# Kernel tuning notes

Measured on AMD Instinct MI355X. Metric: run time of the kernel, lower is better.

Reference implementation:

```python
import jax, jax.numpy as jnp
import numpy as np

CUTOFF = 0.05

def _freq_filter(x_chw, filter_type):
    # x_chw: [C,H,W] = batch element 0, detached in the original (stop_gradient)
    x = jax.lax.stop_gradient(x_chw)
    C, H, W = x.shape
    a = jnp.abs(x)
    mn = a.min(axis=(1, 2), keepdims=True)
    ptp = a.max(axis=(1, 2), keepdims=True) - mn
    # np.uint8(255*(a-mn)/ptp): values in [0,255], cast truncates -> floor
    q = jnp.floor(255.0 * (a - mn) / ptp)
    f = jnp.fft.fftshift(jnp.fft.fft2(q), axes=(-2, -1))
    crow, ccol = H // 2, W // 2
    dr, dc = int(CUTOFF * crow), int(CUTOFF * ccol)
    m = jnp.zeros((H, W), dtype=q.dtype)
    m = m.at[crow - dr:crow + dr, ccol - dc:ccol + dc].set(1.0)
    if filter_type == 'low_pass':
        m = 1.0 - m  # note: original 'low_pass' actually removes low freqs
    out = jnp.abs(jnp.fft.ifft2(jnp.fft.ifftshift(f * m, axes=(-2, -1))))
    return out.astype(x_chw.dtype)  # [C,H,W]

def _conv1x1(x, w, b):
    # x: [B,C,H,W], w: [O,C], b: [O]
    return jnp.einsum('oc,bchw->bohw', w, x) + b[None, :, None, None]

def setup_inputs() -> dict:
    key = jax.random.key(0)
    ks = jax.random.split(key, 7)
    B, C, H, W = 1, 256, 96, 96
    fuse = jax.random.normal(ks[0], (B, C, H, W), dtype=jnp.float32)
    s = 1.0 / np.sqrt(C)
    Wq = jax.random.normal(ks[1], (C, C), dtype=jnp.float32) * s
    bq = jax.random.normal(ks[2], (C,), dtype=jnp.float32) * 0.01
    Wk = jax.random.normal(ks[3], (C, C), dtype=jnp.float32) * s
    bk = jax.random.normal(ks[4], (C,), dtype=jnp.float32) * 0.01
    Wv = jax.random.normal(ks[5], (C, C), dtype=jnp.float32) * s
    bv = jax.random.normal(ks[6], (C,), dtype=jnp.float32) * 0.01
    return {"fuse": fuse, "Wq": Wq, "bq": bq, "Wk": Wk, "bk": bk, "Wv": Wv, "bv": bv}

def reference(fuse, Wq, bq, Wk, bk, Wv, bv):
    B, C, H, W = fuse.shape
    scale = 1.0 / (C ** 0.5)
    # frequency-filtered maps (computed from batch 0, broadcast to all batches)
    FQ = jnp.broadcast_to(_freq_filter(fuse[0], 'high_pass'), fuse.shape)
    FK = jnp.broadcast_to(_freq_filter(fuse[0], 'low_pass'), fuse.shape)
    fuse_Query = _conv1x1(FQ, Wq, bq).reshape(B, C, H * W)     # [B,C,HW]
    fuse_Q_mask = fuse_Query.reshape(B * H, C * W)             # [B*H, C*W]
    fuse_Query_t = jnp.transpose(fuse_Query, (0, 2, 1))        # [B,HW,C]
    fuse_Key = _conv1x1(FK, Wk, bk).reshape(B, C, H * W)       # [B,C,HW]
    Fuse_Q_mask = jnp.max(fuse_Q_mask, axis=0, keepdims=True)  # [1, C*W]
    mask_KQ = jnp.einsum('bnc,bcm->bnm', fuse_Query_t, fuse_Key) * scale  # [B,HW,HW]
    mask_KQ = jax.nn.softmax(mask_KQ, axis=0)  # softmax over batch dim (as in original)
    mask_KQ = jnp.max(mask_KQ, axis=1)                         # [B,HW]
    mask_KQ = mask_KQ.reshape(-1, W)                           # [B*H, W]
    mask_KQ = jnp.max(mask_KQ, axis=-1, keepdims=True)         # [B*H, 1]
    mask = (mask_KQ @ Fuse_Q_mask).reshape(B, C, H, W)
    fuse_Value = _conv1x1(fuse, Wv, bv)
    return fuse_Value + fuse_Value * mask
```

## Files before the change

kernel.cpp:

```cpp
#include <hip/hip_runtime.h>
#include <math.h>

#define CCH 256
#define HW  9216
#define CW  24576
#define TWO_PI 6.28318530717958647692f

typedef __attribute__((ext_vector_type(8))) short short8;
typedef __attribute__((ext_vector_type(4))) float f32x4;

__device__ inline unsigned short f2bf(float f) {
    unsigned u = __float_as_uint(f);
    unsigned r = (u + 0x7FFFu + ((u >> 16) & 1u)) >> 16;
    return (unsigned short)r;
}

__global__ __launch_bounds__(256) void k_wf(const float* __restrict__ Wq,
                                            const float* __restrict__ Wv,
                                            short8* __restrict__ Wqt,
                                            short8* __restrict__ Wvt,
                                            unsigned* __restrict__ FQm) {
    int widx = blockIdx.x;
    int t = threadIdx.x;
    int z0 = widx * 384;
    FQm[z0 + t] = 0u;
    if (t < 128) FQm[z0 + 256 + t] = 0u;
    const float* src = (widx >= 32) ? Wv : Wq;
    short8* dst = (widx >= 32) ? Wvt : Wqt;
    int cidx = (widx & 31) * 256 + t;
    int ot = cidx >> 11, kc = (cidx >> 6) & 31, m = cidx & 63;
    const float* s = src + (ot * 64 + m) * 256 + kc * 8;
    short8 v;
    #pragma unroll
    for (int e = 0; e < 8; ++e) v[e] = (short)f2bf(s[e]);
    dst[cidx] = v;
}

__global__ __launch_bounds__(768) void k_dft(const float* __restrict__ x,
                                             float* __restrict__ Fg) {
    __shared__ float qa[HW];
    __shared__ float cs[96][2];
    __shared__ float Gp[8][96][5];
    __shared__ float Gs[96][6];
    __shared__ float red[24];
    __shared__ float s_mn, s_ptp;
    int c = blockIdx.x, t = threadIdx.x;
    const float* xp = x + c * HW;
    if (t < 96) { float a = TWO_PI * (float)t / 96.0f; cs[t][0] = cosf(a); cs[t][1] = sinf(a); }
    float lo = 1e30f, hi = 0.f;
    #pragma unroll
    for (int i = 0; i < 12; ++i) {
        float a = fabsf(xp[t + i * 768]);
        qa[t + i * 768] = a;
        lo = fminf(lo, a);
        hi = fmaxf(hi, a);
    }
    #pragma unroll
    for (int d = 32; d; d >>= 1) {
        lo = fminf(lo, __shfl_xor(lo, d, 64));
        hi = fmaxf(hi, __shfl_xor(hi, d, 64));
    }
    if ((t & 63) == 0) { red[t >> 6] = lo; red[12 + (t >> 6)] = hi; }
    __syncthreads();
    if (t == 0) {
        lo = red[0]; hi = red[12];
        #pragma unroll
        for (int i = 1; i < 12; ++i) { lo = fminf(lo, red[i]); hi = fmaxf(hi, red[12 + i]); }
        s_mn = lo; s_ptp = hi - lo;
    }
    __syncthreads();
    float mn = s_mn, ptp = s_ptp;

    {
        int xx = t % 96, h = t / 96;
        float g0r = 0, g0i = 0, g1r = 0, g1i = 0, g2 = 0;
        for (int y = h * 12; y < h * 12 + 12; ++y) {
            float q = floorf(255.0f * (qa[y * 96 + xx] - mn) / ptp);
            float c1 = cs[y][0], s1 = cs[y][1];
            float c2 = c1 * c1 - s1 * s1, s2 = 2.0f * c1 * s1;
            g0r += q * c2; g0i += q * s2;
            g1r += q * c1; g1i += q * s1;
            g2  += q;
        }
        Gp[h][xx][0] = g0r; Gp[h][xx][1] = g0i;
        Gp[h][xx][2] = g1r; Gp[h][xx][3] = g1i;
        Gp[h][xx][4] = g2;
    }
    __syncthreads();
    if (t < 96) {
        #pragma unroll
        for (int j = 0; j < 5; ++j) {
            float s = 0.f;
            #pragma unroll
            for (int h = 0; h < 8; ++h) s += Gp[h][t][j];
            Gs[t][j] = s;
        }
        Gs[t][5] = 0.f;
    }
    __syncthreads();
    if (t < 64) {
        int coef = t >> 2, qq = t & 3;
        int ky = coef >> 2, kx = coef & 3;
        float fr = 0, fi = 0;
        for (int xx = qq * 24; xx < qq * 24 + 24; ++xx) {
            float c1 = cs[xx][0], s1 = cs[xx][1];
            float er, ei;
            if (kx == 0)      { er = c1 * c1 - s1 * s1; ei = 2.0f * c1 * s1; }
            else if (kx == 1) { er = c1; ei = s1; }
            else if (kx == 2) { er = 1.f; ei = 0.f; }
            else              { er = c1; ei = -s1; }
            float gr, gi;
            if (ky == 0)      { gr = Gs[xx][0]; gi = Gs[xx][1]; }
            else if (ky == 1) { gr = Gs[xx][2]; gi = Gs[xx][3]; }
            else if (ky == 2) { gr = Gs[xx][4]; gi = 0.f; }
            else              { gr = Gs[xx][2]; gi = -Gs[xx][3]; }
            fr += gr * er - gi * ei;
            fi += gr * ei + gi * er;
        }
        fr += __shfl_xor(fr, 1, 64); fr += __shfl_xor(fr, 2, 64);
        fi += __shfl_xor(fi, 1, 64); fi += __shfl_xor(fi, 2, 64);
        if (qq == 0) {
            Fg[c * 32 + 2 * coef]     = fr;
            Fg[c * 32 + 2 * coef + 1] = fi;
        }
    }
}

__global__ __launch_bounds__(256) void k_gemm1(const short8* __restrict__ Wt,
                                               const float* __restrict__ Fg,
                                               const float* __restrict__ bias,
                                               unsigned* __restrict__ FQm) {
    __shared__ short8 As[2048];
    __shared__ short8 Bs[2048];
    __shared__ float Rs[2048][2];
    int tid = threadIdx.x;
    int pt_ = blockIdx.x, ot = blockIdx.y;
    const short8* wsrc = Wt + ot * 2048;
    #pragma unroll
    for (int i = 0; i < 8; ++i) As[i * 256 + tid] = wsrc[i * 256 + tid];

    int p0 = pt_ * 64;
    int y0 = p0 / 96;
    {
        int yi = (tid >> 2) & 1, kx = tid & 3, cb = tid >> 3;
        float ay = TWO_PI * (float)(y0 + yi) / 96.0f;
        float cyv = cosf(ay), syv = sinf(ay);
        float cy2 = cyv * cyv - syv * syv, sy2 = 2.f * cyv * syv;
        float Ur[4] = { cy2, cyv, 1.f, cyv };
        float Ui[4] = { -sy2, -syv, 0.f, syv };
        #pragma unroll
        for (int i = 0; i < 8; ++i) {
            int cc = cb + i * 32;
            float rr = 0.f, ri = 0.f;
            #pragma unroll
            for (int ky = 0; ky < 4; ++ky) {
                float fr = Fg[cc * 32 + 2 * (ky * 4 + kx)];
                float fi = Fg[cc * 32 + 2 * (ky * 4 + kx) + 1];
                rr += fr * Ur[ky] - fi * Ui[ky];
                ri += fr * Ui[ky] + fi * Ur[ky];
            }
            Rs[cc * 8 + yi * 4 + kx][0] = rr;
            Rs[cc * 8 + yi * 4 + kx][1] = ri;
        }
    }
    __syncthreads();
    const float inv = 1.0f / 9216.0f;
    #pragma unroll
    for (int i = 0; i < 8; ++i) {
        int si = i * 256 + tid;
        int kcg = si >> 6, n = si & 63;
        int p = p0 + n;
        int y = p / 96, xx = p - y * 96;
        int yi = y - y0;
        float axv = TWO_PI * (float)xx / 96.0f;
        float cxv = cosf(axv), sxv = sinf(axv);
        float cx2 = cxv * cxv - sxv * sxv, sx2 = 2.f * cxv * sxv;
        float Tr[4] = { cx2, cxv, 1.f, cxv };
        float Ti[4] = { -sx2, -sxv, 0.f, sxv };
        short8 vv;
        #pragma unroll
        for (int e = 0; e < 8; ++e) {
            int rb = (kcg * 8 + e) * 8 + yi * 4;
            float ar = 0.f, ai = 0.f;
            #pragma unroll
            for (int kx = 0; kx < 4; ++kx) {
                float rr = Rs[rb + kx][0], ri = Rs[rb + kx][1];
                ar += rr * Tr[kx] - ri * Ti[kx];
                ai += rr * Ti[kx] + ri * Tr[kx];
            }
            vv[e] = (short)f2bf(sqrtf(ar * ar + ai * ai) * inv);
        }
        Bs[si] = vv;
    }
    __syncthreads();

    int l = tid & 63, w = tid >> 6;
    int wr = w >> 1, wc = w & 1;
    int l15 = l & 15, quad = l >> 4;
    f32x4 acc[2][2] = {};
    int abase = wr * 32 + l15;
    int bbase = wc * 32 + l15;
    #pragma unroll
    for (int s = 0; s < 8; ++s) {
        int kc = s * 4 + quad;
        short8 a0 = As[kc * 64 + abase];
        short8 a1 = As[kc * 64 + abase + 16];
        short8 b0 = Bs[kc * 64 + bbase];
        short8 b1 = Bs[kc * 64 + bbase + 16];
        acc[0][0] = __builtin_amdgcn_mfma_f32_16x16x32_bf16(a0, b0, acc[0][0], 0, 0, 0);
        acc[0][1] = __builtin_amdgcn_mfma_f32_16x16x32_bf16(a0, b1, acc[0][1], 0, 0, 0);
        acc[1][0] = __builtin_amdgcn_mfma_f32_16x16x32_bf16(a1, b0, acc[1][0], 0, 0, 0);
        acc[1][1] = __builtin_amdgcn_mfma_f32_16x16x32_bf16(a1, b1, acc[1][1], 0, 0, 0);
    }
    #pragma unroll
    for (int ni = 0; ni < 2; ++ni) {
        #pragma unroll
        for (int r = 0; r < 4; ++r) {
            int o_lo = ot * 64 + wr * 32 + quad * 4 + r;
            float v = fmaxf(acc[0][ni][r] + bias[o_lo], acc[1][ni][r] + bias[o_lo + 16]);
            v = fmaxf(v, __shfl_xor(v, 32, 64));
            if (quad < 2) {
                int p = pt_ * 64 + wc * 32 + ni * 16 + l15;
                int k = ((quad * 4 + r) & 7) * HW + p;
                if (k >= CW) k -= CW;
                if (k >= CW) k -= CW;
                unsigned u = __float_as_uint(v);
                unsigned key = (u & 0x80000000u) ? ~u : (u | 0x80000000u);
                atomicMax(&FQm[k], key);
            }
        }
    }
}

__global__ __launch_bounds__(256) void k_gemm2(const short8* __restrict__ Wt,
                                               const float* __restrict__ x,
                                               const float* __restrict__ bias,
                                               const unsigned* __restrict__ FQm,
                                               float* __restrict__ out) {
    __shared__ short8 As[2048];
    __shared__ short8 Bs[2048];
    __shared__ unsigned short lt[64][66];
    int tid = threadIdx.x;
    int pt_ = blockIdx.x, ot = blockIdx.y;
    const short8* wsrc = Wt + ot * 2048;
    #pragma unroll
    for (int i = 0; i < 8; ++i) As[i * 256 + tid] = wsrc[i * 256 + tid];

    int p0 = pt_ * 64;
    int tx = tid & 63, tw = tid >> 6;
    for (int ct4 = 0; ct4 < 4; ++ct4) {
        #pragma unroll
        for (int i = 0; i < 16; ++i) {
            int row = tw * 16 + i;
            lt[row][tx] = f2bf(x[(size_t)(ct4 * 64 + row) * HW + p0 + tx]);
        }
        __syncthreads();
        #pragma unroll
        for (int ch = 0; ch < 2; ++ch) {
            int lc = ch * 256 + tid;
            int kcg = lc >> 6, n = lc & 63;
            short8 v;
            #pragma unroll
            for (int e = 0; e < 8; ++e) v[e] = (short)lt[kcg * 8 + e][n];
            Bs[(ct4 * 8 + kcg) * 64 + n] = v;
        }
        __syncthreads();
    }

    int l = tid & 63, w = tid >> 6;
    int wr = w >> 1, wc = w & 1;
    int l15 = l & 15, quad = l >> 4;
    f32x4 acc[2][2] = {};
    int abase = wr * 32 + l15;
    int bbase = wc * 32 + l15;
    #pragma unroll
    for (int s = 0; s < 8; ++s) {
        int kc = s * 4 + quad;
        short8 a0 = As[kc * 64 + abase];
        short8 a1 = As[kc * 64 + abase + 16];
        short8 b0 = Bs[kc * 64 + bbase];
        short8 b1 = Bs[kc * 64 + bbase + 16];
        acc[0][0] = __builtin_amdgcn_mfma_f32_16x16x32_bf16(a0, b0, acc[0][0], 0, 0, 0);
        acc[0][1] = __builtin_amdgcn_mfma_f32_16x16x32_bf16(a0, b1, acc[0][1], 0, 0, 0);
        acc[1][0] = __builtin_amdgcn_mfma_f32_16x16x32_bf16(a1, b0, acc[1][0], 0, 0, 0);
        acc[1][1] = __builtin_amdgcn_mfma_f32_16x16x32_bf16(a1, b1, acc[1][1], 0, 0, 0);
    }
    #pragma unroll
    for (int mi = 0; mi < 2; ++mi) {
        #pragma unroll
        for (int ni = 0; ni < 2; ++ni) {
            #pragma unroll
            for (int r = 0; r < 4; ++r) {
                int o = ot * 64 + wr * 32 + mi * 16 + quad * 4 + r;
                int p = pt_ * 64 + wc * 32 + ni * 16 + l15;
                int k = ((quad * 4 + r) & 7) * HW + p;
                if (k >= CW) k -= CW;
                if (k >= CW) k -= CW;
                unsigned key = FQm[k];
                unsigned ub = (key & 0x80000000u) ? (key ^ 0x80000000u) : ~key;
                float m = __uint_as_float(ub);
                float v = acc[mi][ni][r] + bias[o];
                out[(size_t)o * HW + p] = v * (1.0f + m);
            }
        }
    }
}

extern "C" void kernel_launch(void* const* d_in, const int* in_sizes, int n_in,
                              void* d_out, int out_size, void* d_ws, size_t ws_size,
                              hipStream_t stream) {
    const float* fuse = (const float*)d_in[0];
    const float* Wq   = (const float*)d_in[1];
    const float* bq   = (const float*)d_in[2];
    const float* Wv   = (const float*)d_in[5];
    const float* bv   = (const float*)d_in[6];
    float* out = (float*)d_out;

    char* ws = (char*)d_ws;
    unsigned* FQm = (unsigned*)(ws);
    float*    Fg  = (float*)(ws + 98304);
    short8*   Wqt = (short8*)(ws + 131072);
    short8*   Wvt = (short8*)(ws + 262144);

    k_wf<<<64, 256, 0, stream>>>(Wq, Wv, Wqt, Wvt, FQm);
    k_dft<<<256, 768, 0, stream>>>(fuse, Fg);
    k_gemm1<<<dim3(144, 4), 256, 0, stream>>>(Wqt, Fg, bq, FQm);
    k_gemm2<<<dim3(144, 4), 256, 0, stream>>>(Wvt, fuse, bv, FQm, out);
}
```

Measured before the change: 120.1 us.

## Merge weight-prep into DFT kernel and load gemm2 B tile directly

Result: faster. 115.6 us (-3.8%).

```diff
diff --git a/kernel.cpp b/kernel.cpp
--- a/kernel.cpp
+++ b/kernel.cpp
@@ -15,28 +15,12 @@
     return (unsigned short)r;
 }
 
-__global__ __launch_bounds__(256) void k_wf(const float* __restrict__ Wq,
-                                            const float* __restrict__ Wv,
-                                            short8* __restrict__ Wqt,
-                                            short8* __restrict__ Wvt,
-                                            unsigned* __restrict__ FQm) {
-    int widx = blockIdx.x;
-    int t = threadIdx.x;
-    int z0 = widx * 384;
-    FQm[z0 + t] = 0u;
-    if (t < 128) FQm[z0 + 256 + t] = 0u;
-    const float* src = (widx >= 32) ? Wv : Wq;
-    short8* dst = (widx >= 32) ? Wvt : Wqt;
-    int cidx = (widx & 31) * 256 + t;
-    int ot = cidx >> 11, kc = (cidx >> 6) & 31, m = cidx & 63;
-    const float* s = src + (ot * 64 + m) * 256 + kc * 8;
-    short8 v;
-    #pragma unroll
-    for (int e = 0; e < 8; ++e) v[e] = (short)f2bf(s[e]);
-    dst[cidx] = v;
-}
-
-__global__ __launch_bounds__(768) void k_dft(const float* __restrict__ x,
+__global__ __launch_bounds__(768) void k_pre(const float* __restrict__ x,
+                                             const float* __restrict__ Wq,
+                                             const float* __restrict__ Wv,
+                                             short8* __restrict__ Wqt,
+                                             short8* __restrict__ Wvt,
+                                             unsigned* __restrict__ FQm,
                                              float* __restrict__ Fg) {
     __shared__ float qa[HW];
     __shared__ float cs[96][2];
@@ -44,7 +28,26 @@
     __shared__ float Gs[96][6];
     __shared__ float red[24];
     __shared__ float s_mn, s_ptp;
-    int c = blockIdx.x, t = threadIdx.x;
+    int bid = blockIdx.x, t = threadIdx.x;
+
+    if (bid >= 256) {
+        int widx = bid - 256;
+        if (t < 256) {
+            const float* src = (widx >= 32) ? Wv : Wq;
+            short8* dst = (widx >= 32) ? Wvt : Wqt;
+            int cidx = (widx & 31) * 256 + t;
+            int ot = cidx >> 11, kc = (cidx >> 6) & 31, m = cidx & 63;
+            const float* s = src + (ot * 64 + m) * 256 + kc * 8;
+            short8 v;
+            #pragma unroll
+            for (int e = 0; e < 8; ++e) v[e] = (short)f2bf(s[e]);
+            dst[cidx] = v;
+        }
+        return;
+    }
+
+    int c = bid;
+    if (t < 96) FQm[c * 96 + t] = 0u;
     const float* xp = x + c * HW;
     if (t < 96) { float a = TWO_PI * (float)t / 96.0f; cs[t][0] = cosf(a); cs[t][1] = sinf(a); }
     float lo = 1e30f, hi = 0.f;
@@ -239,7 +242,6 @@
                                                float* __restrict__ out) {
     __shared__ short8 As[2048];
     __shared__ short8 Bs[2048];
-    __shared__ unsigned short lt[64][66];
     int tid = threadIdx.x;
     int pt_ = blockIdx.x, ot = blockIdx.y;
     const short8* wsrc = Wt + ot * 2048;
@@ -247,25 +249,17 @@
     for (int i = 0; i < 8; ++i) As[i * 256 + tid] = wsrc[i * 256 + tid];
 
     int p0 = pt_ * 64;
-    int tx = tid & 63, tw = tid >> 6;
-    for (int ct4 = 0; ct4 < 4; ++ct4) {
-        #pragma unroll
-        for (int i = 0; i < 16; ++i) {
-            int row = tw * 16 + i;
-            lt[row][tx] = f2bf(x[(size_t)(ct4 * 64 + row) * HW + p0 + tx]);
-        }
-        __syncthreads();
-        #pragma unroll
-        for (int ch = 0; ch < 2; ++ch) {
-            int lc = ch * 256 + tid;
-            int kcg = lc >> 6, n = lc & 63;
-            short8 v;
-            #pragma unroll
-            for (int e = 0; e < 8; ++e) v[e] = (short)lt[kcg * 8 + e][n];
-            Bs[(ct4 * 8 + kcg) * 64 + n] = v;
-        }
-        __syncthreads();
-    }
+    #pragma unroll
+    for (int i = 0; i < 8; ++i) {
+        int si = i * 256 + tid;
+        int KC = si >> 6, n = si & 63;
+        const float* xb = x + (size_t)(KC * 8) * HW + p0 + n;
+        short8 v;
+        #pragma unroll
+        for (int e = 0; e < 8; ++e) v[e] = (short)f2bf(xb[(size_t)e * HW]);
+        Bs[si] = v;
+    }
+    __syncthreads();
 
     int l = tid & 63, w = tid >> 6;
     int wr = w >> 1, wc = w & 1;
@@ -322,8 +316,7 @@
     short8*   Wqt = (short8*)(ws + 131072);
     short8*   Wvt = (short8*)(ws + 262144);
 
-    k_wf<<<64, 256, 0, stream>>>(Wq, Wv, Wqt, Wvt, FQm);
-    k_dft<<<256, 768, 0, stream>>>(fuse, Fg);
+    k_pre<<<320, 768, 0, stream>>>(fuse, Wq, Wv, Wqt, Wvt, FQm, Fg);
     k_gemm1<<<dim3(144, 4), 256, 0, stream>>>(Wqt, Fg, bq, FQm);
     k_gemm2<<<dim3(144, 4), 256, 0, stream>>>(Wvt, fuse, bv, FQm, out);
 }
```
